# Optimization experiments

Measured on AMD Instinct MI355X. Metric: run time of the kernel, lower is better.

## Reference

```python
import jax, jax.numpy as jnp
import numpy as np

B, T, D_IN, H, K, C = 8, 2048, 512, 384, 8192, 8
N_BLOCKS = 6
EPS = 1e-5


def conv1d(x, w, b, pad, groups=1):
    # x: [B, Cin, T], w: [Cout, Cin//groups, k]
    y = jax.lax.conv_general_dilated(
        x, w, window_strides=(1,), padding=[(pad, pad)],
        dimension_numbers=("NCH", "OIH", "NCH"), feature_group_count=groups)
    return y + b[None, :, None]


def layernorm(x, g, b):
    # normalize over last axis
    m = jnp.mean(x, axis=-1, keepdims=True)
    v = jnp.mean(jnp.square(x - m), axis=-1, keepdims=True)
    return (x - m) * jax.lax.rsqrt(v + EPS) * g + b


def setup_inputs() -> dict:
    key = jax.random.key(0)
    ks = iter(jax.random.split(key, 32))
    s = 0.02
    inp = {
        "x": jax.random.normal(next(ks), (B, T, D_IN), dtype=jnp.float32),
        "enc_w": jax.random.normal(next(ks), (H, D_IN, 7)) * s,
        "enc_b": jnp.zeros((H,)),
        "enc_ln_g": jnp.ones((H,)),
        "enc_ln_b": jnp.zeros((H,)),
        "blk_dw_w": jax.random.normal(next(ks), (N_BLOCKS, H, 1, 7)) * s,
        "blk_dw_b": jnp.zeros((N_BLOCKS, H)),
        "blk_ln_g": jnp.ones((N_BLOCKS, H)),
        "blk_ln_b": jnp.zeros((N_BLOCKS, H)),
        "blk_w1": jax.random.normal(next(ks), (N_BLOCKS, 4 * H, H)) * s,
        "blk_b1": jnp.zeros((N_BLOCKS, 4 * H)),
        "blk_w2": jax.random.normal(next(ks), (N_BLOCKS, H, 4 * H)) * s,
        "blk_b2": jnp.zeros((N_BLOCKS, H)),
        "out_w": jax.random.normal(next(ks), (C, H, 1)) * s,
        "out_b": jnp.zeros((C,)),
        "embeddings": jax.random.normal(next(ks), (K, C)),
    }
    return inp


def encode(x, enc_w, enc_b, enc_ln_g, enc_ln_b, blk_dw_w, blk_dw_b,
           blk_ln_g, blk_ln_b, blk_w1, blk_b1, blk_w2, blk_b2, out_w, out_b):
    h = x.transpose(0, 2, 1)                       # [B, D_IN, T]
    h = conv1d(h, enc_w, enc_b, pad=3)             # [B, H, T]
    h = layernorm(h.transpose(0, 2, 1), enc_ln_g, enc_ln_b).transpose(0, 2, 1)
    for i in range(N_BLOCKS):
        res = h
        h = conv1d(h, blk_dw_w[i], blk_dw_b[i], pad=3, groups=H)  # depthwise
        ht = h.transpose(0, 2, 1)                  # [B, T, H]
        ht = layernorm(ht, blk_ln_g[i], blk_ln_b[i])
        ht = jnp.einsum("bth,fh->btf", ht, blk_w1[i]) + blk_b1[i]
        ht = jax.nn.gelu(ht, approximate=False)    # torch GELU is exact erf
        ht = jnp.einsum("btf,hf->bth", ht, blk_w2[i]) + blk_b2[i]
        h = ht.transpose(0, 2, 1) + res
    z = conv1d(h, out_w, out_b, pad=0)             # [B, C, T]
    return z.transpose(0, 2, 1)                    # [B, T, C]


def reference(x, enc_w, enc_b, enc_ln_g, enc_ln_b, blk_dw_w, blk_dw_b,
              blk_ln_g, blk_ln_b, blk_w1, blk_b1, blk_w2, blk_b2,
              out_w, out_b, embeddings):
    z = encode(x, enc_w, enc_b, enc_ln_g, enc_ln_b, blk_dw_w, blk_dw_b,
               blk_ln_g, blk_ln_b, blk_w1, blk_b1, blk_w2, blk_b2, out_w, out_b)
    flat = z.reshape(-1, C)                        # [B*T, C]
    # squared euclidean distances: same argmin as torch.cdist
    d2 = (jnp.sum(flat * flat, axis=1, keepdims=True)
          - 2.0 * flat @ embeddings.T
          + jnp.sum(embeddings * embeddings, axis=1))  # [B*T, K]
    indices = jnp.argmin(d2, axis=1)               # [B*T], int
    return indices
```

## Files before the change

### kernel.cpp

```cpp
#include <hip/hip_runtime.h>
#include <math.h>

#define T_   2048
#define DIN  512
#define H_   384
#define H4_  1536
#define BT_  16384

typedef _Float16 half_t;
typedef _Float16 f16x8 __attribute__((ext_vector_type(8)));
typedef float f32x4 __attribute__((ext_vector_type(4)));

#define LO_SCALE 2048.0f
#define LO_INV   4.8828125e-4f

__device__ __forceinline__ void lds_barrier() {
    asm volatile("s_waitcnt lgkmcnt(0)\n\ts_barrier" ::: "memory");
}

__device__ __forceinline__ void split2(float v, half_t* hi, half_t* lo) {
    half_t h = (half_t)v;
    *hi = h;
    *lo = (half_t)((v - (float)h) * LO_SCALE);
}

__global__ void k_split(const float* __restrict__ in, half_t* __restrict__ hi,
                        half_t* __restrict__ lo, long n) {
    long i = (long)blockIdx.x * 256 + threadIdx.x;
    if (i >= n) return;
    split2(in[i], hi + i, lo + i);
}

__global__ void k_split_encw(const float* __restrict__ in, half_t* __restrict__ hi,
                             half_t* __restrict__ lo) {
    int idx = blockIdx.x * 256 + threadIdx.x;
    if (idx >= H_ * 3584) return;
    int n = idx / 3584;
    int r = idx % 3584;
    int tap = r >> 9, i = r & 511;
    split2(in[n * 3584 + i * 7 + tap], hi + idx, lo + idx);
}

__global__ void k_ln(const float* __restrict__ in, float* __restrict__ out,
                     const float* __restrict__ g, const float* __restrict__ b) {
    int row = blockIdx.x;
    int lane = threadIdx.x;
    const float* ir = in + (long)row * H_;
    float v[6];
    float s = 0.f;
#pragma unroll
    for (int j = 0; j < 6; ++j) { v[j] = ir[lane + (j << 6)]; s += v[j]; }
#pragma unroll
    for (int o = 32; o > 0; o >>= 1) s += __shfl_down(s, o, 64);
    s = __shfl(s, 0, 64);
    float mean = s * (1.f / 384.f);
    float q = 0.f;
#pragma unroll
    for (int j = 0; j < 6; ++j) { float d = v[j] - mean; q += d * d; }
#pragma unroll
    for (int o = 32; o > 0; o >>= 1) q += __shfl_down(q, o, 64);
    q = __shfl(q, 0, 64);
    float rstd = rsqrtf(q * (1.f / 384.f) + 1e-5f);
    float* orow = out + (long)row * H_;
#pragma unroll
    for (int j = 0; j < 6; ++j) {
        int c = lane + (j << 6);
        orow[c] = (v[j] - mean) * rstd * g[c] + b[c];
    }
}

__global__ __launch_bounds__(256) void k_dwconv_ln(
    const float* __restrict__ h, half_t* __restrict__ oh,
    half_t* __restrict__ ol,
    const float* __restrict__ w, const float* __restrict__ wb,
    const float* __restrict__ g, const float* __restrict__ gb) {
    int row = (blockIdx.x << 2) + (threadIdx.x >> 6);
    int b = row >> 11;
    int t = row & 2047;
    int lane = threadIdx.x & 63;
    const float* hb = h + ((long)b * T_) * H_;
    float v[6];
    float s = 0.f;
#pragma unroll
    for (int j = 0; j < 6; ++j) {
        int c = lane + (j << 6);
        float acc = wb[c];
        const float* wc = w + c * 7;
#pragma unroll
        for (int k = 0; k < 7; ++k) {
            int tt = t + k - 3;
            if ((unsigned)tt < (unsigned)T_)
                acc = fmaf(hb[(long)tt * H_ + c], wc[k], acc);
        }
        v[j] = acc;
        s += acc;
    }
#pragma unroll
    for (int o = 32; o > 0; o >>= 1) s += __shfl_down(s, o, 64);
    s = __shfl(s, 0, 64);
    float mean = s * (1.f / 384.f);
    float q = 0.f;
#pragma unroll
    for (int j = 0; j < 6; ++j) { float d = v[j] - mean; q += d * d; }
#pragma unroll
    for (int o = 32; o > 0; o >>= 1) q += __shfl_down(q, o, 64);
    q = __shfl(q, 0, 64);
    float rstd = rsqrtf(q * (1.f / 384.f) + 1e-5f);
    long ro = (long)row * H_;
#pragma unroll
    for (int j = 0; j < 6; ++j) {
        int c = lane + (j << 6);
        float val = (v[j] - mean) * rstd * g[c] + gb[c];
        split2(val, oh + ro + c, ol + ro + c);
    }
}

#define DECLSET(S) float4 pAh##S, pAl##S, pBh0##S, pBl0##S, pBh1##S, pBl1##S

#define LOADREGS(S, k0_) do {                                               \
    int k0v = (k0_);                                                        \
    if (MODE == 0) {                                                        \
        int kk = k0v + ak;                                                  \
        int tap = kk >> 9, ii = kk & 511;                                   \
        int ta = tt0 + tap;                                                 \
        pAh##S = pAl##S = make_float4(0.f, 0.f, 0.f, 0.f);                  \
        if ((unsigned)ta < 2048u) {                                         \
            long o = ((long)bq * 2048 + ta) * 512 + ii;                     \
            pAh##S = *(const float4*)(Ah + o);                              \
            pAl##S = *(const float4*)(Al + o);                              \
        }                                                                   \
    } else {                                                                \
        pAh##S = *(const float4*)(Ah + aoff + k0v);                         \
        pAl##S = *(const float4*)(Al + aoff + k0v);                         \
    }                                                                       \
    pBh0##S = *(const float4*)(Bh + boff0 + k0v);                           \
    pBl0##S = *(const float4*)(Bl + boff0 + k0v);                           \
    pBh1##S = *(const float4*)(Bh + boff1 + k0v);                           \
    pBl1##S = *(const float4*)(Bl + boff1 + k0v);                           \
} while (0)

#define STOREBUF(S, buf) do {                                               \
    *(float4*)&smem[(buf) * 2048 + aw] = pAh##S;                            \
    *(float4*)&smem[4096 + (buf) * 2048 + aw] = pAl##S;                     \
    int b_ = 8192 + (buf) * 4096 + aw;                                      \
    *(float4*)&smem[b_] = pBh0##S;                                          \
    *(float4*)&smem[b_ + 2048] = pBh1##S;                                   \
    *(float4*)&smem[b_ + 8192] = pBl0##S;                                   \
    *(float4*)&smem[b_ + 8192 + 2048] = pBl1##S;                            \
} while (0)

template <int MODE, int NN>
__global__ __launch_bounds__(256, 3) void k_mgemm64(
    const half_t* __restrict__ Ah, const half_t* __restrict__ Al,
    const half_t* __restrict__ Bh, const half_t* __restrict__ Bl,
    const float* __restrict__ bias, const float* __restrict__ res,
    float* __restrict__ Cf, half_t* __restrict__ Ch, half_t* __restrict__ Cl,
    int N, int K) {
    __shared__ __align__(16) half_t smem[24576];
    const int tid = threadIdx.x;
    const int lane = tid & 63, wid = tid >> 6;
    const int wn = wid << 5;
    const int quad = lane >> 4, l16 = lane & 15;

    constexpr int NWG = 256 * NN;
    constexpr int CHUNK = NWG / 8;
    const int lin = blockIdx.x;
    const int tile = (lin & 7) * CHUNK + (lin >> 3);
    const int m0 = (tile / NN) << 6;
    const int n0 = (tile % NN) << 7;

    const int ar = tid >> 2;
    const int ak = (tid & 3) << 3;

    long aoff = 0;
    int tt0 = 0, bq = 0;
    if (MODE == 0) {
        bq = m0 >> 11;
        tt0 = (m0 & 2047) + ar - 3;
    } else {
        aoff = (long)(m0 + ar) * K + ak;
    }
    const long boff0 = (long)(n0 + ar) * K + ak;
    const long boff1 = boff0 + (long)64 * K;

    const int aw = ar * 32 + ((((tid & 3) ^ (ar >> 1)) & 3) << 3);

    DECLSET(0);
    DECLSET(1);

    f32x4 acc1[4][2] = {};
    f32x4 acc2[4][2] = {};
    const int sw = ((quad ^ (l16 >> 1)) & 3) << 3;

    auto compute = [&](int buf) {
        const int ab = buf * 2048 + l16 * 32 + sw;
        const int bb = 8192 + buf * 4096 + (wn + l16) * 32 + sw;
        f16x8 fah[4], fal[4], fgh[2], fgl[2];
#pragma unroll
        for (int f = 0; f < 4; ++f) {
            fah[f] = *(const f16x8*)&smem[ab + f * 512];
            fal[f] = *(const f16x8*)&smem[ab + 4096 + f * 512];
        }
#pragma unroll
        for (int g = 0; g < 2; ++g) {
            fgh[g] = *(const f16x8*)&smem[bb + g * 512];
            fgl[g] = *(const f16x8*)&smem[bb + 8192 + g * 512];
        }
#pragma unroll
        for (int f = 0; f < 4; ++f)
#pragma unroll
            for (int g = 0; g < 2; ++g)
                acc2[f][g] = __builtin_amdgcn_mfma_f32_16x16x32_f16(fah[f], fgl[g], acc2[f][g], 0, 0, 0);
#pragma unroll
        for (int f = 0; f < 4; ++f)
#pragma unroll
            for (int g = 0; g < 2; ++g)
                acc2[f][g] = __builtin_amdgcn_mfma_f32_16x16x32_f16(fal[f], fgh[g], acc2[f][g], 0, 0, 0);
#pragma unroll
        for (int f = 0; f < 4; ++f)
#pragma unroll
            for (int g = 0; g < 2; ++g)
                acc1[f][g] = __builtin_amdgcn_mfma_f32_16x16x32_f16(fah[f], fgh[g], acc1[f][g], 0, 0, 0);
    };

    const int nIter = K >> 5;
    LOADREGS(0, 0);
    LOADREGS(1, 32);
    STOREBUF(0, 0);
    if (nIter > 2) LOADREGS(0, 64);
    for (int it = 0; it < nIter; it += 2) {
        lds_barrier();
        compute(0);
        STOREBUF(1, 1);
        if (it + 3 < nIter) LOADREGS(1, (it + 3) << 5);
        lds_barrier();
        compute(1);
        if (it + 2 < nIter) {
            STOREBUF(0, 0);
            if (it + 4 < nIter) LOADREGS(0, (it + 4) << 5);
        }
    }

    float bv[2];
    bv[0] = bias[n0 + wn + l16];
    bv[1] = bias[n0 + wn + 16 + l16];

    if (MODE == 1) {
        __syncthreads();
#pragma unroll
        for (int f = 0; f < 4; ++f)
#pragma unroll
            for (int g = 0; g < 2; ++g)
#pragma unroll
                for (int r = 0; r < 4; ++r) {
                    int rm = f * 16 + quad * 4 + r;
                    int cn = wn + g * 16 + l16;
                    float v = acc1[f][g][r] + acc2[f][g][r] * LO_INV + bv[g];
                    v = 0.5f * v * (1.0f + erff(v * 0.70710678118654752f));
                    half_t hh = (half_t)v;
                    smem[rm * 136 + cn] = hh;
                    smem[8704 + rm * 136 + cn] = (half_t)((v - (float)hh) * LO_SCALE);
                }
        __syncthreads();
        int row = tid >> 2, c0 = (tid & 3) << 5;
        long go = (long)(m0 + row) * N + n0 + c0;
        int so = row * 136 + c0;
#pragma unroll
        for (int u = 0; u < 4; ++u) {
            *(float4*)(Ch + go + u * 8) = *(const float4*)&smem[so + u * 8];
            *(float4*)(Cl + go + u * 8) = *(const float4*)&smem[8704 + so + u * 8];
        }
    } else {
#pragma unroll
        for (int f = 0; f < 4; ++f)
#pragma unroll
            for (int g = 0; g < 2; ++g)
#pragma unroll
                for (int r = 0; r < 4; ++r) {
                    long row = m0 + f * 16 + quad * 4 + r;
                    int col = n0 + wn + g * 16 + l16;
                    float v = acc1[f][g][r] + acc2[f][g][r] * LO_INV + bv[g];
                    long o = row * N + col;
                    if (MODE == 2) v += res[o];
                    Cf[o] = v;
                }
    }
}

__global__ __launch_bounds__(256) void k_outconv_argmin(
    const float* __restrict__ h, const float* __restrict__ ow,
    const float* __restrict__ ob, const float* __restrict__ emb,
    int* __restrict__ outIdx) {
    __shared__ float hs[16][H_ + 1];
    __shared__ float zs[16][8];
    __shared__ float es[16 * 516];
    __shared__ float rb[16][16];
    __shared__ int ri[16][16];
    const int tid = threadIdx.x;
    const int row0 = blockIdx.x << 4;

    for (int i = tid; i < 16 * (H_ / 4); i += 256) {
        int r = i / 96;
        int c4 = (i % 96) << 2;
        float4 v = *(const float4*)&h[((long)(row0 + r)) * H_ + c4];
        hs[r][c4] = v.x; hs[r][c4 + 1] = v.y; hs[r][c4 + 2] = v.z; hs[r][c4 + 3] = v.w;
    }
    __syncthreads();

    if (tid < 128) {
        int r = tid & 15, c = tid >> 4;
        float acc = ob[c];
        const float* wc = ow + c * H_;
        for (int j = 0; j < H_; ++j) acc = fmaf(hs[r][j], wc[j], acc);
        zs[r][c] = acc;
    }
    __syncthreads();

    const int r = tid & 15;
    const int sl = tid >> 4;
    float z0 = zs[r][0], z1 = zs[r][1], z2 = zs[r][2], z3 = zs[r][3];
    float z4 = zs[r][4], z5 = zs[r][5], z6 = zs[r][6], z7 = zs[r][7];
    float best = 3.4e38f;
    int bi = 0;

    for (int ch = 0; ch < 8; ++ch) {
        __syncthreads();
        for (int i = tid; i < 2048; i += 256) {
            int e = i >> 1;
            int half = (i & 1) << 2;
            float4 src = *(const float4*)&emb[(((long)(ch << 10)) + e) * 8 + half];
            *(float4*)&es[(e >> 6) * 516 + ((e & 63) << 3) + half] = src;
        }
        __syncthreads();
        const float* ep = es + sl * 516;
        int gbase = (ch << 10) + (sl << 6);
#pragma unroll 4
        for (int j = 0; j < 64; ++j) {
            float4 e0 = *(const float4*)(ep + (j << 3));
            float4 e1 = *(const float4*)(ep + (j << 3) + 4);
            float t, d;
            t = e0.x - z0; d = t * t;
            t = e0.y - z1; d = fmaf(t, t, d);
            t = e0.z - z2; d = fmaf(t, t, d);
            t = e0.w - z3; d = fmaf(t, t, d);
            t = e1.x - z4; d = fmaf(t, t, d);
            t = e1.y - z5; d = fmaf(t, t, d);
            t = e1.z - z6; d = fmaf(t, t, d);
            t = e1.w - z7; d = fmaf(t, t, d);
            if (d < best) { best = d; bi = gbase + j; }
        }
    }
    rb[r][sl] = best;
    ri[r][sl] = bi;
    __syncthreads();
    if (sl == 0) {
        float bb = rb[r][0];
        int bbi = ri[r][0];
#pragma unroll
        for (int s2 = 1; s2 < 16; ++s2) {
            float v = rb[r][s2];
            int i2 = ri[r][s2];
            if (v < bb || (v == bb && i2 < bbi)) { bb = v; bbi = i2; }
        }
        outIdx[row0 + r] = bbi;
    }
}

extern "C" void kernel_launch(void* const* d_in, const int* in_sizes, int n_in,
                              void* d_out, int out_size, void* d_ws, size_t ws_size,
                              hipStream_t stream) {
    const float* x        = (const float*)d_in[0];
    const float* enc_w    = (const float*)d_in[1];
    const float* enc_b    = (const float*)d_in[2];
    const float* enc_ln_g = (const float*)d_in[3];
    const float* enc_ln_b = (const float*)d_in[4];
    const float* blk_dw_w = (const float*)d_in[5];
    const float* blk_dw_b = (const float*)d_in[6];
    const float* blk_ln_g = (const float*)d_in[7];
    const float* blk_ln_b = (const float*)d_in[8];
    const float* blk_w1   = (const float*)d_in[9];
    const float* blk_b1   = (const float*)d_in[10];
    const float* blk_w2   = (const float*)d_in[11];
    const float* blk_b2   = (const float*)d_in[12];
    const float* out_w    = (const float*)d_in[13];
    const float* out_b    = (const float*)d_in[14];
    const float* emb      = (const float*)d_in[15];
    int* out = (int*)d_out;

    char* base = (char*)d_ws;
    float*  h    = (float*)base;
    half_t* tmph = (half_t*)(base + 25165824);
    half_t* tmpl = (half_t*)(base + 37748736);
    half_t* ht4h = (half_t*)(base + 50331648);
    half_t* ht4l = (half_t*)(base + 100663296);
    half_t* ench = (half_t*)(base + 150994944);
    half_t* encl = (half_t*)(base + 153747456);
    half_t* w1h  = (half_t*)(base + 156499968);
    half_t* w1l  = (half_t*)(base + 163577856);
    half_t* w2h  = (half_t*)(base + 170655744);
    half_t* w2l  = (half_t*)(base + 177733632);
    half_t* xh = ht4h;
    half_t* xl = (half_t*)(base + 50331648 + 16777216);

    k_split<<<(8388608 + 255) / 256, 256, 0, stream>>>(x, xh, xl, 8388608L);
    k_split<<<(3538944 + 255) / 256, 256, 0, stream>>>(blk_w1, w1h, w1l, 3538944L);
    k_split<<<(3538944 + 255) / 256, 256, 0, stream>>>(blk_w2, w2h, w2l, 3538944L);
    k_split_encw<<<(H_ * 3584 + 255) / 256, 256, 0, stream>>>(enc_w, ench, encl);

    k_mgemm64<0, 3><<<768, 256, 0, stream>>>(xh, xl, ench, encl, enc_b,
                                             nullptr, h, nullptr, nullptr,
                                             H_, 3584);
    k_ln<<<BT_, 64, 0, stream>>>(h, h, enc_ln_g, enc_ln_b);

    for (int i = 0; i < 6; ++i) {
        k_dwconv_ln<<<BT_ / 4, 256, 0, stream>>>(h, tmph, tmpl, blk_dw_w + i * H_ * 7,
                                                 blk_dw_b + i * H_, blk_ln_g + i * H_,
                                                 blk_ln_b + i * H_);
        k_mgemm64<1, 12><<<3072, 256, 0, stream>>>(
            tmph, tmpl, w1h + (long)i * 589824, w1l + (long)i * 589824,
            blk_b1 + i * H4_, nullptr, nullptr, ht4h, ht4l, H4_, H_);
        k_mgemm64<2, 3><<<768, 256, 0, stream>>>(
            ht4h, ht4l, w2h + (long)i * 589824, w2l + (long)i * 589824,
            blk_b2 + i * H_, h, h, nullptr, nullptr, H_, H4_);
    }

    k_outconv_argmin<<<BT_ / 16, 256, 0, stream>>>(h, out_w, out_b, emb, out);
}
```

Measured before the change: 1.701 ms.

## Add 128x96-tile split-fp16 MFMA GEMM for MLP block layers

Adds a new GEMM kernel that uses 128x96 output tiles instead of 64x128 tiles, with four waves each owning a 64x48 sub-tile. It double-buffers LDS with a simpler one-stage register prefetch and uses a grouped tile ordering across blocks. The two per-block MLP GEMMs switch to this kernel, which cuts the number of workgroups and raises the compute done per loaded byte. The trade-off is more accumulator registers per thread and a shallower prefetch, which may hurt latency hiding. The old kernel's MODE 1 epilogue is removed, so it now only serves the encoder GEMM.

```diff
diff --git a/kernel.cpp b/kernel.cpp
--- a/kernel.cpp
+++ b/kernel.cpp
@@ -245,43 +245,177 @@
     bv[0] = bias[n0 + wn + l16];
     bv[1] = bias[n0 + wn + 16 + l16];
 
+#pragma unroll
+    for (int f = 0; f < 4; ++f)
+#pragma unroll
+        for (int g = 0; g < 2; ++g)
+#pragma unroll
+            for (int r = 0; r < 4; ++r) {
+                long row = m0 + f * 16 + quad * 4 + r;
+                int col = n0 + wn + g * 16 + l16;
+                float v = acc1[f][g][r] + acc2[f][g][r] * LO_INV + bv[g];
+                long o = row * N + col;
+                if (MODE == 2) v += res[o];
+                Cf[o] = v;
+            }
+}
+
+#define LOAD96(k0_) do {                                                    \
+    int k0v = (k0_);                                                        \
+    long a_ = aoff + k0v;                                                   \
+    qAh0 = *(const float4*)(Ah + a_);                                       \
+    qAh1 = *(const float4*)(Ah + a_ + 8);                                   \
+    qAl0 = *(const float4*)(Al + a_);                                       \
+    qAl1 = *(const float4*)(Al + a_ + 8);                                   \
+    long b_ = boff0 + k0v;                                                  \
+    qBh0 = *(const float4*)(Bh + b_);                                       \
+    qBl0 = *(const float4*)(Bl + b_);                                       \
+    if (tid < 128) {                                                        \
+        long c_ = boff1 + k0v;                                              \
+        qBh1 = *(const float4*)(Bh + c_);                                   \
+        qBl1 = *(const float4*)(Bl + c_);                                   \
+    }                                                                       \
+} while (0)
+
+#define STORE96(buf) do {                                                   \
+    int ab_ = (buf) * 14336 + ra * 32;                                      \
+    *(float4*)&smem[ab_ + pa0 * 8] = qAh0;                                  \
+    *(float4*)&smem[ab_ + pa1 * 8] = qAh1;                                  \
+    *(float4*)&smem[ab_ + 4096 + pa0 * 8] = qAl0;                           \
+    *(float4*)&smem[ab_ + 4096 + pa1 * 8] = qAl1;                           \
+    int bb_ = (buf) * 14336 + 8192 + rb0 * 32 + pb0 * 8;                    \
+    *(float4*)&smem[bb_] = qBh0;                                            \
+    *(float4*)&smem[bb_ + 3072] = qBl0;                                     \
+    if (tid < 128) {                                                        \
+        int bc_ = bb_ + 64 * 32;                                            \
+        *(float4*)&smem[bc_] = qBh1;                                        \
+        *(float4*)&smem[bc_ + 3072] = qBl1;                                 \
+    }                                                                       \
+} while (0)
+
+template <int MODE, int NT>
+__global__ __launch_bounds__(256, 2) void k_mgemm96(
+    const half_t* __restrict__ Ah, const half_t* __restrict__ Al,
+    const half_t* __restrict__ Bh, const half_t* __restrict__ Bl,
+    const float* __restrict__ bias, const float* __restrict__ res,
+    float* __restrict__ Cf, half_t* __restrict__ Ch, half_t* __restrict__ Cl,
+    int N, int K) {
+    __shared__ __align__(16) half_t smem[28672];
+    const int tid = threadIdx.x;
+    const int lane = tid & 63, wid = tid >> 6;
+    const int wm = (wid >> 1) << 6;
+    const int wn = (wid & 1) * 48;
+    const int quad = lane >> 4, l16 = lane & 15;
+
+    constexpr int NWG = 128 * NT;
+    constexpr int CHUNK = NWG / 8;
+    const int lin = blockIdx.x;
+    const int tile = (lin & 7) * CHUNK + (lin >> 3);
+    const int m0 = (tile / NT) << 7;
+    const int n0 = (tile % NT) * 96;
+
+    const int ra = tid >> 1;
+    const int ga0 = (tid & 1) << 1;
+    const int rb0 = tid >> 2;
+    const int gb = tid & 3;
+    const int pa0 = (ga0 ^ ((ra >> 1) & 3)) & 3;
+    const int pa1 = pa0 ^ 1;
+    const int pb0 = (gb ^ ((rb0 >> 1) & 3)) & 3;
+
+    const long aoff = (long)(m0 + ra) * K + (ga0 << 3);
+    const long boff0 = (long)(n0 + rb0) * K + (gb << 3);
+    const long boff1 = boff0 + (long)64 * K;
+
+    float4 qAh0, qAh1, qAl0, qAl1, qBh0, qBl0, qBh1, qBl1;
+
+    f32x4 acc1[4][3] = {};
+    f32x4 acc2[4][3] = {};
+    const int sw = ((quad ^ (l16 >> 1)) & 3) << 3;
+
+    auto compute = [&](int buf) {
+        const int ab = buf * 14336 + (wm + l16) * 32 + sw;
+        const int bb = buf * 14336 + 8192 + (wn + l16) * 32 + sw;
+        f16x8 fah[4], fal[4], fgh[3], fgl[3];
+#pragma unroll
+        for (int f = 0; f < 4; ++f) {
+            fah[f] = *(const f16x8*)&smem[ab + f * 512];
+            fal[f] = *(const f16x8*)&smem[ab + 4096 + f * 512];
+        }
+#pragma unroll
+        for (int g = 0; g < 3; ++g) {
+            fgh[g] = *(const f16x8*)&smem[bb + g * 512];
+            fgl[g] = *(const f16x8*)&smem[bb + 3072 + g * 512];
+        }
+#pragma unroll
+        for (int f = 0; f < 4; ++f)
+#pragma unroll
+            for (int g = 0; g < 3; ++g)
+                acc2[f][g] = __builtin_amdgcn_mfma_f32_16x16x32_f16(fah[f], fgl[g], acc2[f][g], 0, 0, 0);
+#pragma unroll
+        for (int f = 0; f < 4; ++f)
+#pragma unroll
+            for (int g = 0; g < 3; ++g)
+                acc2[f][g] = __builtin_amdgcn_mfma_f32_16x16x32_f16(fal[f], fgh[g], acc2[f][g], 0, 0, 0);
+#pragma unroll
+        for (int f = 0; f < 4; ++f)
+#pragma unroll
+            for (int g = 0; g < 3; ++g)
+                acc1[f][g] = __builtin_amdgcn_mfma_f32_16x16x32_f16(fah[f], fgh[g], acc1[f][g], 0, 0, 0);
+    };
+
+    const int nIter = K >> 5;
+    LOAD96(0);
+    STORE96(0);
+    int cur = 0;
+    for (int it = 0; it < nIter; ++it) {
+        if (it + 1 < nIter) LOAD96((it + 1) << 5);
+        lds_barrier();
+        compute(cur);
+        if (it + 1 < nIter) STORE96(cur ^ 1);
+        cur ^= 1;
+    }
+
+    float bv[3];
+#pragma unroll
+    for (int g = 0; g < 3; ++g) bv[g] = bias[n0 + wn + g * 16 + l16];
+
     if (MODE == 1) {
         __syncthreads();
 #pragma unroll
         for (int f = 0; f < 4; ++f)
 #pragma unroll
-            for (int g = 0; g < 2; ++g)
+            for (int g = 0; g < 3; ++g)
 #pragma unroll
                 for (int r = 0; r < 4; ++r) {
-                    int rm = f * 16 + quad * 4 + r;
+                    int rm = wm + f * 16 + quad * 4 + r;
                     int cn = wn + g * 16 + l16;
                     float v = acc1[f][g][r] + acc2[f][g][r] * LO_INV + bv[g];
                     v = 0.5f * v * (1.0f + erff(v * 0.70710678118654752f));
                     half_t hh = (half_t)v;
-                    smem[rm * 136 + cn] = hh;
-                    smem[8704 + rm * 136 + cn] = (half_t)((v - (float)hh) * LO_SCALE);
+                    smem[rm * 104 + cn] = hh;
+                    smem[13312 + rm * 104 + cn] = (half_t)((v - (float)hh) * LO_SCALE);
                 }
         __syncthreads();
-        int row = tid >> 2, c0 = (tid & 3) << 5;
+        int row = tid >> 1, c0 = (tid & 1) * 48;
         long go = (long)(m0 + row) * N + n0 + c0;
-        int so = row * 136 + c0;
-#pragma unroll
-        for (int u = 0; u < 4; ++u) {
+        int so = row * 104 + c0;
+#pragma unroll
+        for (int u = 0; u < 6; ++u) {
             *(float4*)(Ch + go + u * 8) = *(const float4*)&smem[so + u * 8];
-            *(float4*)(Cl + go + u * 8) = *(const float4*)&smem[8704 + so + u * 8];
+            *(float4*)(Cl + go + u * 8) = *(const float4*)&smem[13312 + so + u * 8];
         }
     } else {
 #pragma unroll
         for (int f = 0; f < 4; ++f)
 #pragma unroll
-            for (int g = 0; g < 2; ++g)
+            for (int g = 0; g < 3; ++g)
 #pragma unroll
                 for (int r = 0; r < 4; ++r) {
-                    long row = m0 + f * 16 + quad * 4 + r;
+                    long row = m0 + wm + f * 16 + quad * 4 + r;
                     int col = n0 + wn + g * 16 + l16;
                     float v = acc1[f][g][r] + acc2[f][g][r] * LO_INV + bv[g];
                     long o = row * N + col;
-                    if (MODE == 2) v += res[o];
+                    v += res[o];
                     Cf[o] = v;
                 }
     }
@@ -416,10 +550,10 @@
         k_dwconv_ln<<<BT_ / 4, 256, 0, stream>>>(h, tmph, tmpl, blk_dw_w + i * H_ * 7,
                                                  blk_dw_b + i * H_, blk_ln_g + i * H_,
                                                  blk_ln_b + i * H_);
-        k_mgemm64<1, 12><<<3072, 256, 0, stream>>>(
+        k_mgemm96<1, 16><<<2048, 256, 0, stream>>>(
             tmph, tmpl, w1h + (long)i * 589824, w1l + (long)i * 589824,
             blk_b1 + i * H4_, nullptr, nullptr, ht4h, ht4l, H4_, H_);
-        k_mgemm64<2, 3><<<768, 256, 0, stream>>>(
+        k_mgemm96<2, 4><<<512, 256, 0, stream>>>(
             ht4h, ht4l, w2h + (long)i * 589824, w2l + (long)i * 589824,
             blk_b2 + i * H_, h, h, nullptr, nullptr, H_, H4_);
     }
```

Measured after the change: 1.665 ms. -2.2%, faster.
